# Kernel optimization log

Hardware: AMD Instinct MI355X
Metric: run time of the kernel (lower is better)

The kernel has to match this reference:

```python
import jax, jax.numpy as jnp
import numpy as np

DIM = 1024
GRID_SIZE = 5
SPLINE_ORDER = 3
N_TOKENS = 8192
EPS = 1e-6


def setup_inputs() -> dict:
    key = jax.random.key(0)
    k1, k2, k3 = jax.random.split(key, 3)
    x = jax.random.normal(k1, (N_TOKENS, DIM), dtype=jnp.float32)
    norm_weight = jnp.ones((DIM,), dtype=jnp.float32)
    # nn.Linear default init ~ U(-1/sqrt(dim), 1/sqrt(dim)); randn scaled is fine for a numeric baseline
    base_weight = jax.random.normal(k2, (DIM, DIM), dtype=jnp.float32) * (1.0 / np.sqrt(DIM))
    spline_weight = jax.random.normal(k3, (DIM, GRID_SIZE), dtype=jnp.float32) * 0.1
    gamma = jnp.full((DIM,), 1e-5, dtype=jnp.float32)
    return {"x": x, "norm_weight": norm_weight, "base_weight": base_weight,
            "spline_weight": spline_weight, "gamma": gamma}


def _knots():
    h = 2.0 / GRID_SIZE
    n_knots = GRID_SIZE + SPLINE_ORDER + 1
    return jnp.linspace(-1.0 - SPLINE_ORDER * h, 1.0 + SPLINE_ORDER * h, n_knots)


def _b_spline_basis(x_clamped, knots):
    # x_clamped: (N, D) -> bases: (N, D, grid_size)
    xe = x_clamped[..., None]  # (N, D, 1)
    bases = ((xe >= knots[:-1]) & (xe < knots[1:])).astype(x_clamped.dtype)
    for k in range(1, SPLINE_ORDER + 1):  # fixed small unroll (Cox-de Boor)
        n = bases.shape[-1] - 1
        left_den = jnp.maximum(knots[k:k + n] - knots[:n], 1e-8)
        left = (xe - knots[:n]) / left_den * bases[..., :n]
        right_den = jnp.maximum(knots[k + 1:k + 1 + n] - knots[1:1 + n], 1e-8)
        right = (knots[k + 1:k + 1 + n] - xe) / right_den * bases[..., 1:1 + n]
        bases = left + right
    return bases


def reference(x, norm_weight, base_weight, spline_weight, gamma):
    knots = _knots()
    # RMSNorm
    xf = x.astype(jnp.float32)
    x_norm = (xf * jax.lax.rsqrt(jnp.mean(xf * xf, axis=-1, keepdims=True) + EPS)).astype(x.dtype)
    x_norm = x_norm * norm_weight
    # base path: Linear(dim, dim, bias=False) -> x @ W.T
    base_out = x_norm @ base_weight.T
    # spline path
    x_clamped = jnp.clip(x_norm, -1.0, 1.0)
    spline_bases = _b_spline_basis(x_clamped, knots)  # (N, D, grid_size)
    spline_out = jnp.einsum('ndb,db->nd', spline_bases, spline_weight)
    return x + (base_out + spline_out) * gamma
```

## Files before the change

### kernel.cpp

```cpp
#include <hip/hip_runtime.h>
#include <hip/hip_bf16.h>
#include <stdint.h>

#define DIM 1024
#define NTOK 8192

#define BM 128
#define BN 128
#define BKB 64

typedef unsigned char uchar;
typedef __attribute__((ext_vector_type(4)))  int   i32x4;
typedef __attribute__((ext_vector_type(8)))  int   i32x8;
typedef __attribute__((ext_vector_type(16))) float f32x16;

#define SCALE_A 0x7E7E7E7Eu
#define SCALE_B 0x79797979u

#define GLOAD_LDS16(g, l)                                                \
    __builtin_amdgcn_global_load_lds(                                    \
        (const __attribute__((address_space(1))) void*)(g),              \
        (__attribute__((address_space(3))) void*)(l), 16, 0, 0)

__device__ __forceinline__ unsigned short f2bf(float f) {
    union { float f; uint32_t u; } v; v.f = f;
    uint32_t u = v.u;
    u += 0x7FFFu + ((u >> 16) & 1u);
    return (unsigned short)(u >> 16);
}
__device__ __forceinline__ float bf2f(unsigned short h) {
    union { uint32_t u; float f; } v; v.u = ((uint32_t)h) << 16; return v.f;
}

__device__ __forceinline__ float spline_eval(float xn, float s0, float s1,
                                             float s2, float s3, float s4) {
    const float xc = fminf(fmaxf(xn, -1.0f), 1.0f);
    const float u = (xc + 2.2f) * (1.0f / 0.55f);
    int j = (int)u;
    j = j < 2 ? 2 : (j > 5 ? 5 : j);
    const float t = u - (float)j;
    const float omt = 1.0f - t;
    const float t2 = t * t, t3 = t2 * t;
    const float w0 = omt * omt * omt * (1.0f / 6.0f);
    const float w1 = (3.0f * t3 - 6.0f * t2 + 4.0f) * (1.0f / 6.0f);
    const float w2 = (-3.0f * t3 + 3.0f * t2 + 3.0f * t + 1.0f) * (1.0f / 6.0f);
    const float w3 = t3 * (1.0f / 6.0f);
    float so;
    if (j == 2)      so = w1 * s0 + w2 * s1 + w3 * s2;
    else if (j == 3) so = w0 * s0 + w1 * s1 + w2 * s2 + w3 * s3;
    else if (j == 4) so = w0 * s1 + w1 * s2 + w2 * s3 + w3 * s4;
    else             so = w0 * s2 + w1 * s3 + w2 * s4;
    return so;
}

__device__ __forceinline__ uint32_t fp4e(float v) {
    const float a = fabsf(v);
    uint32_t c = a < 0.25f ? 0u : a < 0.75f ? 1u : a < 1.25f ? 2u
               : a < 1.75f ? 3u : a < 2.5f  ? 4u : a < 3.5f  ? 5u
               : a < 5.0f  ? 6u : 7u;
    return c | ((__float_as_uint(v) >> 28) & 8u);
}
__device__ __forceinline__ uint32_t pack8_fp4(float v0, float v1, float v2, float v3,
                                              float v4, float v5, float v6, float v7) {
    return  fp4e(v0)        | (fp4e(v1) << 4)  | (fp4e(v2) << 8)  | (fp4e(v3) << 12)
         | (fp4e(v4) << 16) | (fp4e(v5) << 20) | (fp4e(v6) << 24) | (fp4e(v7) << 28);
}

__global__ __launch_bounds__(256) void prep_kernel(
    const float* __restrict__ x, const float* __restrict__ nw,
    const float* __restrict__ W,
    uchar* __restrict__ A4, uchar* __restrict__ B4,
    float* __restrict__ rr)
{
    const int bid = blockIdx.x;
    const int t = threadIdx.x;
    const int lane = t & 63, w = t >> 6;

    if (bid >= NTOK / 4) {
        const int row = (bid - NTOK / 4) * 4 + w;
        const float4* src = reinterpret_cast<const float4*>(W + (size_t)row * DIM) + lane * 4;
        const float4 a = src[0], b = src[1], c = src[2], d = src[3];
        uint2 o;
        o.x = pack8_fp4(a.x*64.f, a.y*64.f, a.z*64.f, a.w*64.f,
                        b.x*64.f, b.y*64.f, b.z*64.f, b.w*64.f);
        o.y = pack8_fp4(c.x*64.f, c.y*64.f, c.z*64.f, c.w*64.f,
                        d.x*64.f, d.y*64.f, d.z*64.f, d.w*64.f);
        reinterpret_cast<uint2*>(B4 + (size_t)row * (DIM / 2))[lane] = o;
        return;
    }

    const int row = bid * 4 + w;
    const float4* xr = reinterpret_cast<const float4*>(x + (size_t)row * DIM) + lane * 4;
    const float4 a = xr[0], b = xr[1], c = xr[2], d = xr[3];

    float ssq = a.x*a.x + a.y*a.y + a.z*a.z + a.w*a.w
              + b.x*b.x + b.y*b.y + b.z*b.z + b.w*b.w
              + c.x*c.x + c.y*c.y + c.z*c.z + c.w*c.w
              + d.x*d.x + d.y*d.y + d.z*d.z + d.w*d.w;
    #pragma unroll
    for (int off = 32; off; off >>= 1) ssq += __shfl_xor(ssq, off, 64);

    const float r = rsqrtf(ssq * (1.0f / DIM) + 1e-6f);
    if (lane == 0) rr[row] = r;

    const float4* nwr = reinterpret_cast<const float4*>(nw) + lane * 4;
    const float4 na = nwr[0], nb = nwr[1], nc = nwr[2], nd = nwr[3];
    const float r2 = 2.0f * r;
    uint2 o;
    o.x = pack8_fp4(a.x*r2*na.x, a.y*r2*na.y, a.z*r2*na.z, a.w*r2*na.w,
                    b.x*r2*nb.x, b.y*r2*nb.y, b.z*r2*nb.z, b.w*r2*nb.w);
    o.y = pack8_fp4(c.x*r2*nc.x, c.y*r2*nc.y, c.z*r2*nc.z, c.w*r2*nc.w,
                    d.x*r2*nd.x, d.y*r2*nd.y, d.z*r2*nd.z, d.w*r2*nd.w);
    reinterpret_cast<uint2*>(A4 + (size_t)row * (DIM / 2))[lane] = o;
}

__global__ __launch_bounds__(512, 4) void gemm_ep_kernel(
    const uchar* __restrict__ A,
    const uchar* __restrict__ B,
    const float* __restrict__ x,
    const float* __restrict__ rrow,
    const float* __restrict__ nw,
    const float* __restrict__ sw,
    const float* __restrict__ gamma,
    float* __restrict__ out)
{
    __shared__ uchar SB[4 * 16384];

    const int tid = threadIdx.x;
    const int lane = tid & 63, wid = tid >> 6;

    const int bid = blockIdx.x;
    const int swz = (bid & 7) * 64 + (bid >> 3);
    const int bm = swz >> 3, bn = swz & 7;

    const int wm = wid >> 1, wn = wid & 1;

    f32x16 acc[2] = {};

    const int srow = tid >> 2;
    const int scol = ((tid & 3) ^ ((tid >> 3) & 3)) * 16;
    const uchar* Ag = A + (size_t)(bm * BM + srow) * (DIM / 2) + scol;
    const uchar* Bg = B + (size_t)(bn * BN + srow) * (DIM / 2) + scol;
    const int oA = tid * 16;
    const int oB = 8192 + tid * 16;

    const int xorv = (lane >> 1) & 3;
    const int p0 = (lane >> 5) ^ xorv;
    const int aBase = (wm * 32 + (lane & 31)) * 64;
    const int bBase = 8192 + (wn * 64 + (lane & 31)) * 64;

#define STAGE(bi, kt) do {                                           \
        uchar* sb_ = SB + (bi) * 16384;                              \
        GLOAD_LDS16(Ag + (size_t)(kt) * BKB, sb_ + oA);              \
        GLOAD_LDS16(Bg + (size_t)(kt) * BKB, sb_ + oB);              \
    } while (0)

#define MK8(v) ((i32x8){(v)[0], (v)[1], (v)[2], (v)[3], 0, 0, 0, 0})

#define COMP(bi) do {                                                \
        const uchar* sb_ = SB + (bi) * 16384;                        \
        const i32x4 a0  = *reinterpret_cast<const i32x4*>(sb_ + aBase + p0 * 16);        \
        const i32x4 a1  = *reinterpret_cast<const i32x4*>(sb_ + aBase + (p0 ^ 2) * 16);  \
        const i32x4 b00 = *reinterpret_cast<const i32x4*>(sb_ + bBase + p0 * 16);        \
        const i32x4 b01 = *reinterpret_cast<const i32x4*>(sb_ + bBase + 2048 + p0 * 16); \
        const i32x4 b10 = *reinterpret_cast<const i32x4*>(sb_ + bBase + (p0 ^ 2) * 16);  \
        const i32x4 b11 = *reinterpret_cast<const i32x4*>(sb_ + bBase + 2048 + (p0 ^ 2) * 16); \
        acc[0] = __builtin_amdgcn_mfma_scale_f32_32x32x64_f8f6f4(    \
            MK8(a0), MK8(b00), acc[0], 4, 4, 0, SCALE_A, 0, SCALE_B); \
        acc[1] = __builtin_amdgcn_mfma_scale_f32_32x32x64_f8f6f4(    \
            MK8(a0), MK8(b01), acc[1], 4, 4, 0, SCALE_A, 0, SCALE_B); \
        acc[0] = __builtin_amdgcn_mfma_scale_f32_32x32x64_f8f6f4(    \
            MK8(a1), MK8(b10), acc[0], 4, 4, 0, SCALE_A, 0, SCALE_B); \
        acc[1] = __builtin_amdgcn_mfma_scale_f32_32x32x64_f8f6f4(    \
            MK8(a1), MK8(b11), acc[1], 4, 4, 0, SCALE_A, 0, SCALE_B); \
    } while (0)

#define W4v asm volatile("s_waitcnt vmcnt(4)" ::: "memory")
#define W2v asm volatile("s_waitcnt vmcnt(2)" ::: "memory")
#define W0v asm volatile("s_waitcnt vmcnt(0)" ::: "memory")
#define BAR __builtin_amdgcn_s_barrier()

    STAGE(0, 0);
    STAGE(1, 1);
    STAGE(2, 2); W4v; BAR; COMP(0);
    STAGE(3, 3); W4v; BAR; COMP(1);
    STAGE(0, 4); W4v; BAR; COMP(2);
    STAGE(1, 5); W4v; BAR; COMP(3);
    STAGE(2, 6); W4v; BAR; COMP(0);
    STAGE(3, 7); W4v; BAR; COMP(1);
    W2v; BAR; COMP(2);
    W0v; BAR; COMP(3);
    __syncthreads();

#undef STAGE
#undef MK8
#undef COMP
#undef W4v
#undef W2v
#undef W0v
#undef BAR

    unsigned short* Cb = reinterpret_cast<unsigned short*>(SB);
    {
        const int crow0 = wm * 32 + 4 * (lane >> 5);
        const int ccol0 = wn * 64 + (lane & 31);
        #pragma unroll
        for (int j = 0; j < 2; ++j)
            #pragma unroll
            for (int r = 0; r < 16; ++r) {
                const int lr = crow0 + (r & 3) + 8 * (r >> 2);
                Cb[lr * 136 + ccol0 + j * 32] = f2bf(acc[j][r]);
            }
    }
    __syncthreads();

    const int colg = bn * BN + (tid & 31) * 4;
    float sf[20];
    {
        const float4* swp = reinterpret_cast<const float4*>(sw + (size_t)colg * 5);
        #pragma unroll
        for (int q = 0; q < 5; ++q) {
            const float4 w4 = swp[q];
            sf[q * 4 + 0] = w4.x; sf[q * 4 + 1] = w4.y;
            sf[q * 4 + 2] = w4.z; sf[q * 4 + 3] = w4.w;
        }
    }
    const float4 gv  = *reinterpret_cast<const float4*>(gamma + colg);
    const float4 nwv = *reinterpret_cast<const float4*>(nw + colg);

    #pragma unroll
    for (int v = 0; v < 8; ++v) {
        const int lr = (tid >> 5) * 8 + v;
        const size_t grow = (size_t)(bm * BM + lr);
        const ushort4 cb4 = *reinterpret_cast<const ushort4*>(&Cb[lr * 136 + (tid & 31) * 4]);
        const float4 xv = *reinterpret_cast<const float4*>(x + grow * DIM + colg);
        const float rv = rrow[grow];
        float4 ov;
        ov.x = xv.x + (bf2f(cb4.x) + spline_eval(xv.x * rv * nwv.x, sf[0],  sf[1],  sf[2],  sf[3],  sf[4]))  * gv.x;
        ov.y = xv.y + (bf2f(cb4.y) + spline_eval(xv.y * rv * nwv.y, sf[5],  sf[6],  sf[7],  sf[8],  sf[9]))  * gv.y;
        ov.z = xv.z + (bf2f(cb4.z) + spline_eval(xv.z * rv * nwv.z, sf[10], sf[11], sf[12], sf[13], sf[14])) * gv.z;
        ov.w = xv.w + (bf2f(cb4.w) + spline_eval(xv.w * rv * nwv.w, sf[15], sf[16], sf[17], sf[18], sf[19])) * gv.w;
        *reinterpret_cast<float4*>(out + grow * DIM + colg) = ov;
    }
}

extern "C" void kernel_launch(void* const* d_in, const int* in_sizes, int n_in,
                              void* d_out, int out_size, void* d_ws, size_t ws_size,
                              hipStream_t stream) {
    const float* x     = (const float*)d_in[0];
    const float* nw    = (const float*)d_in[1];
    const float* W     = (const float*)d_in[2];
    const float* sw    = (const float*)d_in[3];
    const float* gamma = (const float*)d_in[4];
    float* out = (float*)d_out;

    uchar* A4 = (uchar*)d_ws;
    uchar* B4 = A4 + (size_t)NTOK * (DIM / 2);
    float* rr = (float*)(B4 + (size_t)DIM * (DIM / 2));

    prep_kernel<<<dim3(NTOK / 4 + DIM / 4), 256, 0, stream>>>(x, nw, W, A4, B4, rr);
    gemm_ep_kernel<<<dim3((NTOK / BM) * (DIM / BN)), dim3(512), 0, stream>>>(
        A4, B4, x, rr, nw, sw, gamma, out);
}
```

Baseline: 39.62 us.

## Double GEMM block to 1024 threads with one 32x32 tile per wave

Raises the fused GEMM+epilogue block from 8 to 16 waves. Each wave now computes a single 32x32 accumulator, and each thread issues one global-to-LDS load per stage instead of two (A and B are split across the two halves of the block). The epilogue handles 4 rows per thread instead of 8. The aim is more latency hiding and more parallelism in the epilogue, at the cost of lower per-wave data reuse (LDS reads per MFMA go up) and barriers across 16 waves.

```diff
diff --git a/kernel.cpp b/kernel.cpp
--- a/kernel.cpp
+++ b/kernel.cpp
@@ -114,7 +114,7 @@
     reinterpret_cast<uint2*>(A4 + (size_t)row * (DIM / 2))[lane] = o;
 }
 
-__global__ __launch_bounds__(512, 4) void gemm_ep_kernel(
+__global__ __launch_bounds__(1024, 2) void gemm_ep_kernel(
     const uchar* __restrict__ A,
     const uchar* __restrict__ B,
     const float* __restrict__ x,
@@ -133,84 +133,75 @@
     const int swz = (bid & 7) * 64 + (bid >> 3);
     const int bm = swz >> 3, bn = swz & 7;
 
-    const int wm = wid >> 1, wn = wid & 1;
-
-    f32x16 acc[2] = {};
-
-    const int srow = tid >> 2;
-    const int scol = ((tid & 3) ^ ((tid >> 3) & 3)) * 16;
-    const uchar* Ag = A + (size_t)(bm * BM + srow) * (DIM / 2) + scol;
-    const uchar* Bg = B + (size_t)(bn * BN + srow) * (DIM / 2) + scol;
-    const int oA = tid * 16;
-    const int oB = 8192 + tid * 16;
+    const int wm = wid >> 2, wn = wid & 3;
+
+    f32x16 acc = {};
+
+    const int s = tid & 511;
+    const int srow = s >> 2;
+    const int scol = ((s & 3) ^ ((s >> 3) & 3)) * 16;
+    const uchar* Gsrc = (tid < 512)
+        ? A + (size_t)(bm * BM + srow) * (DIM / 2) + scol
+        : B + (size_t)(bn * BN + srow) * (DIM / 2) + scol;
+    const int oS = (tid < 512 ? 0 : 8192) + s * 16;
 
     const int xorv = (lane >> 1) & 3;
     const int p0 = (lane >> 5) ^ xorv;
     const int aBase = (wm * 32 + (lane & 31)) * 64;
-    const int bBase = 8192 + (wn * 64 + (lane & 31)) * 64;
+    const int bBase = 8192 + (wn * 32 + (lane & 31)) * 64;
 
 #define STAGE(bi, kt) do {                                           \
-        uchar* sb_ = SB + (bi) * 16384;                              \
-        GLOAD_LDS16(Ag + (size_t)(kt) * BKB, sb_ + oA);              \
-        GLOAD_LDS16(Bg + (size_t)(kt) * BKB, sb_ + oB);              \
+        GLOAD_LDS16(Gsrc + (size_t)(kt) * BKB, SB + (bi) * 16384 + oS); \
     } while (0)
 
 #define MK8(v) ((i32x8){(v)[0], (v)[1], (v)[2], (v)[3], 0, 0, 0, 0})
 
 #define COMP(bi) do {                                                \
         const uchar* sb_ = SB + (bi) * 16384;                        \
-        const i32x4 a0  = *reinterpret_cast<const i32x4*>(sb_ + aBase + p0 * 16);        \
-        const i32x4 a1  = *reinterpret_cast<const i32x4*>(sb_ + aBase + (p0 ^ 2) * 16);  \
-        const i32x4 b00 = *reinterpret_cast<const i32x4*>(sb_ + bBase + p0 * 16);        \
-        const i32x4 b01 = *reinterpret_cast<const i32x4*>(sb_ + bBase + 2048 + p0 * 16); \
-        const i32x4 b10 = *reinterpret_cast<const i32x4*>(sb_ + bBase + (p0 ^ 2) * 16);  \
-        const i32x4 b11 = *reinterpret_cast<const i32x4*>(sb_ + bBase + 2048 + (p0 ^ 2) * 16); \
-        acc[0] = __builtin_amdgcn_mfma_scale_f32_32x32x64_f8f6f4(    \
-            MK8(a0), MK8(b00), acc[0], 4, 4, 0, SCALE_A, 0, SCALE_B); \
-        acc[1] = __builtin_amdgcn_mfma_scale_f32_32x32x64_f8f6f4(    \
-            MK8(a0), MK8(b01), acc[1], 4, 4, 0, SCALE_A, 0, SCALE_B); \
-        acc[0] = __builtin_amdgcn_mfma_scale_f32_32x32x64_f8f6f4(    \
-            MK8(a1), MK8(b10), acc[0], 4, 4, 0, SCALE_A, 0, SCALE_B); \
-        acc[1] = __builtin_amdgcn_mfma_scale_f32_32x32x64_f8f6f4(    \
-            MK8(a1), MK8(b11), acc[1], 4, 4, 0, SCALE_A, 0, SCALE_B); \
+        const i32x4 a0 = *reinterpret_cast<const i32x4*>(sb_ + aBase + p0 * 16);       \
+        const i32x4 b0 = *reinterpret_cast<const i32x4*>(sb_ + bBase + p0 * 16);       \
+        const i32x4 a1 = *reinterpret_cast<const i32x4*>(sb_ + aBase + (p0 ^ 2) * 16); \
+        const i32x4 b1 = *reinterpret_cast<const i32x4*>(sb_ + bBase + (p0 ^ 2) * 16); \
+        acc = __builtin_amdgcn_mfma_scale_f32_32x32x64_f8f6f4(       \
+            MK8(a0), MK8(b0), acc, 4, 4, 0, SCALE_A, 0, SCALE_B);    \
+        acc = __builtin_amdgcn_mfma_scale_f32_32x32x64_f8f6f4(       \
+            MK8(a1), MK8(b1), acc, 4, 4, 0, SCALE_A, 0, SCALE_B);    \
     } while (0)
 
-#define W4v asm volatile("s_waitcnt vmcnt(4)" ::: "memory")
 #define W2v asm volatile("s_waitcnt vmcnt(2)" ::: "memory")
+#define W1v asm volatile("s_waitcnt vmcnt(1)" ::: "memory")
 #define W0v asm volatile("s_waitcnt vmcnt(0)" ::: "memory")
 #define BAR __builtin_amdgcn_s_barrier()
 
     STAGE(0, 0);
     STAGE(1, 1);
-    STAGE(2, 2); W4v; BAR; COMP(0);
-    STAGE(3, 3); W4v; BAR; COMP(1);
-    STAGE(0, 4); W4v; BAR; COMP(2);
-    STAGE(1, 5); W4v; BAR; COMP(3);
-    STAGE(2, 6); W4v; BAR; COMP(0);
-    STAGE(3, 7); W4v; BAR; COMP(1);
-    W2v; BAR; COMP(2);
+    STAGE(2, 2); W2v; BAR; COMP(0);
+    STAGE(3, 3); W2v; BAR; COMP(1);
+    STAGE(0, 4); W2v; BAR; COMP(2);
+    STAGE(1, 5); W2v; BAR; COMP(3);
+    STAGE(2, 6); W2v; BAR; COMP(0);
+    STAGE(3, 7); W2v; BAR; COMP(1);
+    W1v; BAR; COMP(2);
     W0v; BAR; COMP(3);
     __syncthreads();
 
 #undef STAGE
 #undef MK8
 #undef COMP
-#undef W4v
 #undef W2v
+#undef W1v
 #undef W0v
 #undef BAR
 
     unsigned short* Cb = reinterpret_cast<unsigned short*>(SB);
     {
         const int crow0 = wm * 32 + 4 * (lane >> 5);
-        const int ccol0 = wn * 64 + (lane & 31);
+        const int ccol0 = wn * 32 + (lane & 31);
         #pragma unroll
-        for (int j = 0; j < 2; ++j)
-            #pragma unroll
-            for (int r = 0; r < 16; ++r) {
-                const int lr = crow0 + (r & 3) + 8 * (r >> 2);
-                Cb[lr * 136 + ccol0 + j * 32] = f2bf(acc[j][r]);
-            }
+        for (int r = 0; r < 16; ++r) {
+            const int lr = crow0 + (r & 3) + 8 * (r >> 2);
+            Cb[lr * 136 + ccol0] = f2bf(acc[r]);
+        }
     }
     __syncthreads();
 
@@ -229,8 +220,8 @@
     const float4 nwv = *reinterpret_cast<const float4*>(nw + colg);
 
     #pragma unroll
-    for (int v = 0; v < 8; ++v) {
-        const int lr = (tid >> 5) * 8 + v;
+    for (int v = 0; v < 4; ++v) {
+        const int lr = (tid >> 5) * 4 + v;
         const size_t grow = (size_t)(bm * BM + lr);
         const ushort4 cb4 = *reinterpret_cast<const ushort4*>(&Cb[lr * 136 + (tid & 31) * 4]);
         const float4 xv = *reinterpret_cast<const float4*>(x + grow * DIM + colg);
@@ -259,6 +250,6 @@
     float* rr = (float*)(B4 + (size_t)DIM * (DIM / 2));
 
     prep_kernel<<<dim3(NTOK / 4 + DIM / 4), 256, 0, stream>>>(x, nw, W, A4, B4, rr);
-    gemm_ep_kernel<<<dim3((NTOK / BM) * (DIM / BN)), dim3(512), 0, stream>>>(
+    gemm_ep_kernel<<<dim3((NTOK / BM) * (DIM / BN)), dim3(1024), 0, stream>>>(
         A4, B4, x, rr, nw, sw, gamma, out);
 }
```

New measurement: 39.29 us. No clear change (-0.8%).
